# Performance work log

Measured on AMD Instinct MI355X. Metric: run time of the kernel, lower is better.

The kernel has to match this reference:

```python
import jax, jax.numpy as jnp
import numpy as np


def _quat_to_rotT(q):
    # q: [..., 4] in (w, x, y, z) order, exactly mirroring the torch entry order,
    # including the final transpose(3, 2). Returns [..., 3, 3].
    w, x, y, z = q[..., 0], q[..., 1], q[..., 2], q[..., 3]
    R = jnp.stack([
        1.0 - 2.0 * (y ** 2 + z ** 2), 2.0 * x * y - 2.0 * w * z, 2.0 * w * y + 2.0 * x * z,
        2.0 * x * y + 2.0 * z * w, 1.0 - 2.0 * (x ** 2 + z ** 2), -2.0 * w * x + 2.0 * y * z,
        -2.0 * w * y + 2.0 * x * z, 2.0 * w * x + 2.0 * y * z, 1.0 - 2.0 * (x ** 2 + y ** 2),
    ], axis=-1).reshape(q.shape[:-1] + (3, 3))
    return jnp.swapaxes(R, -1, -2)


def _forward(pred_t, pred_r, pred_c, target_r, target_t, model_points, choose, symmetric, diameters, rot_anchors):
    bs, num_rot, _ = pred_r.shape
    # --- anchor regularization: cos_dist = bmm(pred_r, rot_anchors^T) ---
    cos_dist = jnp.einsum('brq,aq->bra', pred_r, rot_anchors)  # [bs, R, R]
    diag = jnp.diagonal(cos_dist, axis1=1, axis2=2)             # [bs, R]
    reg = jnp.max(cos_dist, axis=2) - diag
    loss_reg = jnp.mean(jnp.where(reg > 0.001, reg, 0.0))       # F.threshold(x, 0.001, 0)

    # --- rotate model points by every anchor-refined rotation ---
    rotT = _quat_to_rotT(pred_r)                                 # [bs, R, 3, 3]
    mp = model_points[:, 0]                                      # [bs, N, 3]
    pred_pts = jnp.einsum('bnk,brkj->brnj', mp, rotT)            # [bs, R, N, 3]
    tgt = target_r[:, 0]                                         # [bs, M, 3]

    # symmetric branch: pairwise distances via the |a|^2+|b|^2-2ab expansion
    # (avoids materializing the [bs,R,N,M,3] difference tensor; dist tensor only)
    a2 = jnp.sum(pred_pts ** 2, axis=-1)                         # [bs, R, N]
    b2 = jnp.sum(tgt ** 2, axis=-1)                              # [bs, M]
    ab = jnp.einsum('brnk,bmk->brnm', pred_pts, tgt)             # [bs, R, N, M]
    d2 = a2[:, :, :, None] + b2[:, None, None, :] - 2.0 * ab
    dist_pair = jnp.sqrt(jnp.maximum(d2, 1e-12))
    sym_d = jnp.mean(jnp.min(dist_pair, axis=3), axis=2)         # [bs, R]

    # non-symmetric branch: pointwise distance (M == N)
    nonsym_d = jnp.mean(
        jnp.linalg.norm(pred_pts - tgt[:, None, :, :], axis=-1), axis=2)  # [bs, R]

    d = jnp.where(symmetric[:, None], sym_d, nonsym_d)           # [bs, R]
    per_anchor = d / (diameters[:, None] * pred_c) + jnp.log(pred_c)
    loss_r = jnp.sum(jnp.mean(per_anchor, axis=1))               # summed over batch (torch +=)

    # --- translation smooth-L1 against sampled dense field ---
    tflat = jnp.transpose(target_t, (0, 2, 3, 1)).reshape(bs, -1, 3)      # [bs, H*W, 3]
    tsamp = jnp.take_along_axis(tflat, choose[:, :, None], axis=1)        # [bs, n_sel, 3]
    diff_t = pred_t - tsamp
    ad = jnp.abs(diff_t)
    loss_t = jnp.mean(jnp.where(ad < 1.0, 0.5 * diff_t ** 2, ad - 0.5))

    total = loss_r + 2.0 * loss_reg + 5.0 * loss_t
    return total, loss_r, loss_reg, loss_t


def setup_inputs() -> dict:
    key = jax.random.key(0)
    ks = jax.random.split(key, 8)
    bs, num_rot, N, H, W = 8, 60, 500, 80, 80
    pred_t = jax.random.normal(ks[0], (bs, N, 3), jnp.float32)
    pred_r = jax.random.normal(ks[1], (bs, num_rot, 4), jnp.float32)
    pred_c = jax.random.uniform(ks[2], (bs, num_rot), jnp.float32, 0.05, 1.0)
    target_r = jax.random.normal(ks[3], (bs, 1, N, 3), jnp.float32)
    target_t = jax.random.normal(ks[4], (bs, 3, H, W), jnp.float32)
    model_points = jax.random.normal(ks[5], (bs, 1, N, 3), jnp.float32)
    choose = jax.random.randint(ks[6], (bs, N), 0, H * W)
    symmetric = jnp.ones((bs,), dtype=bool)
    diameters = jnp.ones((bs,), jnp.float32)
    rot_anchors = jax.random.normal(ks[7], (num_rot, 4), jnp.float32)
    return {
        'pred_t': pred_t, 'pred_r': pred_r, 'pred_c': pred_c,
        'target_r': target_r, 'target_t': target_t, 'model_points': model_points,
        'choose': choose, 'symmetric': symmetric, 'diameters': diameters,
        'rot_anchors': rot_anchors,
    }


def reference(pred_t, pred_r, pred_c, target_r, target_t, model_points, choose, symmetric, diameters, rot_anchors):
    return _forward(pred_t, pred_r, pred_c, target_r, target_t, model_points,
                    choose, symmetric, diameters, rot_anchors)
```

## Files before the change

kernel.cpp:

```cpp
#include <hip/hip_runtime.h>
#include <math.h>

#define BS 8
#define NR 60
#define NP 500
#define NHW 6400
#define NBLK (BS*NR)
#define NT_ELEMS (BS*NP*3)
#define LT_PER_BLK 25

__global__ __launch_bounds__(256) void main_kernel(
    const float* __restrict__ pred_t,
    const float* __restrict__ pred_r,
    const float* __restrict__ target_r,
    const float* __restrict__ target_t,
    const float* __restrict__ model_points,
    const int*   __restrict__ choose,
    const float* __restrict__ rot_anchors,
    float* __restrict__ out_sym,
    float* __restrict__ out_non,
    float* __restrict__ out_reg,
    float* __restrict__ out_lt)
{
    const int bid = blockIdx.x;
    const int b = bid / NR;
    const int r = bid % NR;
    const int tid = threadIdx.x;

    __shared__ float4 t4s[NP];
    __shared__ float red[8];

    for (int i = tid; i < NP; i += 256) {
        const float* p = target_r + (b * NP + i) * 3;
        float x = p[0], y = p[1], z = p[2];
        t4s[i] = make_float4(x, y, z, x * x + y * y + z * z);
    }

    const float* q = pred_r + bid * 4;
    const float w = q[0], x = q[1], y = q[2], z = q[3];
    const float r00 = 1.f - 2.f * (y * y + z * z);
    const float r01 = 2.f * x * y - 2.f * w * z;
    const float r02 = 2.f * w * y + 2.f * x * z;
    const float r10 = 2.f * x * y + 2.f * z * w;
    const float r11 = 1.f - 2.f * (x * x + z * z);
    const float r12 = -2.f * w * x + 2.f * y * z;
    const float r20 = -2.f * w * y + 2.f * x * z;
    const float r21 = 2.f * w * x + 2.f * y * z;
    const float r22 = 1.f - 2.f * (x * x + y * y);

    float lt = 0.f;
    if (tid < LT_PER_BLK) {
        int e = bid * LT_PER_BLK + tid;
        int bb = e / 1500;
        int rem = e - bb * 1500;
        int n = rem / 3;
        int k = rem - n * 3;
        int pos = choose[bb * NP + n];
        float ts = target_t[(bb * 3 + k) * NHW + pos];
        float diff = pred_t[e] - ts;
        float ad = fabsf(diff);
        lt = (ad < 1.f) ? 0.5f * diff * diff : ad - 0.5f;
    }

    if (tid < 64) {
        float dot = -3.4e38f;
        if (tid < NR) {
            const float* an = rot_anchors + tid * 4;
            dot = w * an[0] + x * an[1] + y * an[2] + z * an[3];
        }
        float diag = __shfl(dot, r, 64);
        float mx = dot;
        for (int o = 32; o > 0; o >>= 1) mx = fmaxf(mx, __shfl_down(mx, o, 64));
        for (int o = 32; o > 0; o >>= 1) lt += __shfl_down(lt, o, 64);
        if (tid == 0) {
            float rg = mx - diag;
            out_reg[bid] = (rg > 0.001f) ? rg : 0.f;
            out_lt[bid] = lt;
        }
    }

    const int n0 = tid;
    const int n1 = tid + 256;
    const bool has1 = (n1 < NP);

    const float* mpb = model_points + b * NP * 3;
    float m0x = mpb[n0 * 3 + 0], m0y = mpb[n0 * 3 + 1], m0z = mpb[n0 * 3 + 2];
    float m1x = 0.f, m1y = 0.f, m1z = 0.f;
    if (has1) { m1x = mpb[n1 * 3 + 0]; m1y = mpb[n1 * 3 + 1]; m1z = mpb[n1 * 3 + 2]; }

    const float p0x = r00 * m0x + r01 * m0y + r02 * m0z;
    const float p0y = r10 * m0x + r11 * m0y + r12 * m0z;
    const float p0z = r20 * m0x + r21 * m0y + r22 * m0z;
    const float p1x = r00 * m1x + r01 * m1y + r02 * m1z;
    const float p1y = r10 * m1x + r11 * m1y + r12 * m1z;
    const float p1z = r20 * m1x + r21 * m1y + r22 * m1z;
    const float a20 = p0x * p0x + p0y * p0y + p0z * p0z;
    const float a21 = p1x * p1x + p1y * p1y + p1z * p1z;

    __syncthreads();

    float mn0A = 3.4e38f, mn0B = 3.4e38f, mn0C = 3.4e38f, mn0D = 3.4e38f;
    float mn1A = 3.4e38f, mn1B = 3.4e38f, mn1C = 3.4e38f, mn1D = 3.4e38f;
    for (int m = 0; m < NP; m += 4) {
        float4 tA = t4s[m + 0];
        float4 tB = t4s[m + 1];
        float4 tC = t4s[m + 2];
        float4 tD = t4s[m + 3];
        float d0A = fmaf(p0x, tA.x, fmaf(p0y, tA.y, p0z * tA.z));
        float d0B = fmaf(p0x, tB.x, fmaf(p0y, tB.y, p0z * tB.z));
        float d0C = fmaf(p0x, tC.x, fmaf(p0y, tC.y, p0z * tC.z));
        float d0D = fmaf(p0x, tD.x, fmaf(p0y, tD.y, p0z * tD.z));
        float d1A = fmaf(p1x, tA.x, fmaf(p1y, tA.y, p1z * tA.z));
        float d1B = fmaf(p1x, tB.x, fmaf(p1y, tB.y, p1z * tB.z));
        float d1C = fmaf(p1x, tC.x, fmaf(p1y, tC.y, p1z * tC.z));
        float d1D = fmaf(p1x, tD.x, fmaf(p1y, tD.y, p1z * tD.z));
        mn0A = fminf(mn0A, fmaf(-2.f, d0A, tA.w));
        mn0B = fminf(mn0B, fmaf(-2.f, d0B, tB.w));
        mn0C = fminf(mn0C, fmaf(-2.f, d0C, tC.w));
        mn0D = fminf(mn0D, fmaf(-2.f, d0D, tD.w));
        mn1A = fminf(mn1A, fmaf(-2.f, d1A, tA.w));
        mn1B = fminf(mn1B, fmaf(-2.f, d1B, tB.w));
        mn1C = fminf(mn1C, fmaf(-2.f, d1C, tC.w));
        mn1D = fminf(mn1D, fmaf(-2.f, d1D, tD.w));
    }
    const float mn0 = fminf(fminf(mn0A, mn0B), fminf(mn0C, mn0D));
    const float mn1 = fminf(fminf(mn1A, mn1B), fminf(mn1C, mn1D));

    float ssym = 0.f, snon = 0.f;
    {
        float d2 = fmaxf(a20 + mn0, 1e-12f);
        ssym += sqrtf(d2);
        float4 t = t4s[n0];
        float dx = p0x - t.x, dy = p0y - t.y, dz = p0z - t.z;
        snon += sqrtf(dx * dx + dy * dy + dz * dz);
    }
    if (has1) {
        float d2 = fmaxf(a21 + mn1, 1e-12f);
        ssym += sqrtf(d2);
        float4 t = t4s[n1];
        float dx = p1x - t.x, dy = p1y - t.y, dz = p1z - t.z;
        snon += sqrtf(dx * dx + dy * dy + dz * dz);
    }

    for (int o = 32; o > 0; o >>= 1) {
        ssym += __shfl_down(ssym, o, 64);
        snon += __shfl_down(snon, o, 64);
    }
    const int wv = tid >> 6, ln = tid & 63;
    if (ln == 0) { red[wv] = ssym; red[4 + wv] = snon; }
    __syncthreads();
    if (tid == 0) {
        out_sym[bid] = red[0] + red[1] + red[2] + red[3];
        out_non[bid] = red[4] + red[5] + red[6] + red[7];
    }
}

__global__ __launch_bounds__(256) void finalize_kernel(
    const float* __restrict__ out_sym, const float* __restrict__ out_non,
    const float* __restrict__ out_reg, const float* __restrict__ out_lt,
    const float* __restrict__ pred_c,
    const unsigned char* __restrict__ symU8, const int* __restrict__ symI,
    const float* __restrict__ diam, float* __restrict__ out)
{
    const int tid = threadIdx.x;
    float s_r = 0.f, s_reg = 0.f, s_t = 0.f;
    for (int i = tid; i < NBLK; i += 256) {
        int b = i / NR;
        bool sym = (symU8[b] != 0) || (symI[b] != 0);
        float sum = sym ? out_sym[i] : out_non[i];
        float d = sum * (1.0f / NP);
        float c = pred_c[i];
        s_r += (d / (diam[b] * c) + logf(c)) * (1.0f / NR);
        s_reg += out_reg[i];
        s_t += out_lt[i];
    }
    __shared__ float red[12];
    for (int o = 32; o > 0; o >>= 1) {
        s_r += __shfl_down(s_r, o, 64);
        s_reg += __shfl_down(s_reg, o, 64);
        s_t += __shfl_down(s_t, o, 64);
    }
    const int wv = tid >> 6, ln = tid & 63;
    if (ln == 0) { red[wv] = s_r; red[4 + wv] = s_reg; red[8 + wv] = s_t; }
    __syncthreads();
    if (tid == 0) {
        float lr = red[0] + red[1] + red[2] + red[3];
        float lreg = (red[4] + red[5] + red[6] + red[7]) * (1.0f / NBLK);
        float ltv = (red[8] + red[9] + red[10] + red[11]) * (1.0f / NT_ELEMS);
        out[0] = lr + 2.f * lreg + 5.f * ltv;
        out[1] = lr;
        out[2] = lreg;
        out[3] = ltv;
    }
}

extern "C" void kernel_launch(void* const* d_in, const int* in_sizes, int n_in,
                              void* d_out, int out_size, void* d_ws, size_t ws_size,
                              hipStream_t stream) {
    const float* pred_t       = (const float*)d_in[0];
    const float* pred_r       = (const float*)d_in[1];
    const float* pred_c       = (const float*)d_in[2];
    const float* target_r     = (const float*)d_in[3];
    const float* target_t     = (const float*)d_in[4];
    const float* model_points = (const float*)d_in[5];
    const int*   choose       = (const int*)d_in[6];
    const unsigned char* symU8 = (const unsigned char*)d_in[7];
    const int*   symI         = (const int*)d_in[7];
    const float* diam         = (const float*)d_in[8];
    const float* anchors      = (const float*)d_in[9];
    float* out = (float*)d_out;

    char* ws = (char*)d_ws;
    float* o_sym = (float*)ws;
    float* o_non = o_sym + NBLK;
    float* o_reg = o_non + NBLK;
    float* o_lt  = o_reg + NBLK;

    main_kernel<<<NBLK, 256, 0, stream>>>(pred_t, pred_r, target_r, target_t,
                                          model_points, choose, anchors,
                                          o_sym, o_non, o_reg, o_lt);
    finalize_kernel<<<1, 256, 0, stream>>>(o_sym, o_non, o_reg, o_lt,
                                           pred_c, symU8, symI, diam, out);
}
```

Before: 95.47 us.

## Process two rotations per block to reuse shared target loads

Each block now handles a pair of rotation hypotheses instead of one, so every float4 target point read from shared memory feeds four distance candidates rather than two. The grid shrinks from 480 to 240 blocks, and the reg and translation-loss work is redistributed to match. This cuts LDS traffic and the per-block setup cost per rotation. The price is fewer blocks than the MI355X's compute units and more registers per thread.

```diff
diff --git a/kernel.cpp b/kernel.cpp
--- a/kernel.cpp
+++ b/kernel.cpp
@@ -3,11 +3,15 @@
 
 #define BS 8
 #define NR 60
+#define NRP 30
 #define NP 500
 #define NHW 6400
-#define NBLK (BS*NR)
+#define NPAIR (BS*NR)
+#define NBLK (BS*NRP)
 #define NT_ELEMS (BS*NP*3)
-#define LT_PER_BLK 25
+#define LT_PER_BLK 50
+
+#define BIGF 3.4e38f
 
 __global__ __launch_bounds__(256) void main_kernel(
     const float* __restrict__ pred_t,
@@ -23,12 +27,14 @@
     float* __restrict__ out_lt)
 {
     const int bid = blockIdx.x;
-    const int b = bid / NR;
-    const int r = bid % NR;
+    const int b  = bid / NRP;
+    const int rp = bid % NRP;
+    const int r0 = 2 * rp, r1 = 2 * rp + 1;
+    const int pair0 = b * NR + r0;
     const int tid = threadIdx.x;
 
     __shared__ float4 t4s[NP];
-    __shared__ float red[8];
+    __shared__ float red[16];
 
     for (int i = tid; i < NP; i += 256) {
         const float* p = target_r + (b * NP + i) * 3;
@@ -36,17 +42,29 @@
         t4s[i] = make_float4(x, y, z, x * x + y * y + z * z);
     }
 
-    const float* q = pred_r + bid * 4;
-    const float w = q[0], x = q[1], y = q[2], z = q[3];
-    const float r00 = 1.f - 2.f * (y * y + z * z);
-    const float r01 = 2.f * x * y - 2.f * w * z;
-    const float r02 = 2.f * w * y + 2.f * x * z;
-    const float r10 = 2.f * x * y + 2.f * z * w;
-    const float r11 = 1.f - 2.f * (x * x + z * z);
-    const float r12 = -2.f * w * x + 2.f * y * z;
-    const float r20 = -2.f * w * y + 2.f * x * z;
-    const float r21 = 2.f * w * x + 2.f * y * z;
-    const float r22 = 1.f - 2.f * (x * x + y * y);
+    const float* q0p = pred_r + pair0 * 4;
+    const float w0 = q0p[0], x0 = q0p[1], y0 = q0p[2], z0 = q0p[3];
+    const float w1 = q0p[4], x1 = q0p[5], y1 = q0p[6], z1 = q0p[7];
+
+    const float A00 = 1.f - 2.f * (y0 * y0 + z0 * z0);
+    const float A01 = 2.f * x0 * y0 - 2.f * w0 * z0;
+    const float A02 = 2.f * w0 * y0 + 2.f * x0 * z0;
+    const float A10 = 2.f * x0 * y0 + 2.f * z0 * w0;
+    const float A11 = 1.f - 2.f * (x0 * x0 + z0 * z0);
+    const float A12 = -2.f * w0 * x0 + 2.f * y0 * z0;
+    const float A20 = -2.f * w0 * y0 + 2.f * x0 * z0;
+    const float A21 = 2.f * w0 * x0 + 2.f * y0 * z0;
+    const float A22 = 1.f - 2.f * (x0 * x0 + y0 * y0);
+
+    const float B00 = 1.f - 2.f * (y1 * y1 + z1 * z1);
+    const float B01 = 2.f * x1 * y1 - 2.f * w1 * z1;
+    const float B02 = 2.f * w1 * y1 + 2.f * x1 * z1;
+    const float B10 = 2.f * x1 * y1 + 2.f * z1 * w1;
+    const float B11 = 1.f - 2.f * (x1 * x1 + z1 * z1);
+    const float B12 = -2.f * w1 * x1 + 2.f * y1 * z1;
+    const float B20 = -2.f * w1 * y1 + 2.f * x1 * z1;
+    const float B21 = 2.f * w1 * x1 + 2.f * y1 * z1;
+    const float B22 = 1.f - 2.f * (x1 * x1 + y1 * y1);
 
     float lt = 0.f;
     if (tid < LT_PER_BLK) {
@@ -63,95 +81,115 @@
     }
 
     if (tid < 64) {
-        float dot = -3.4e38f;
+        float dot = -BIGF;
         if (tid < NR) {
             const float* an = rot_anchors + tid * 4;
-            dot = w * an[0] + x * an[1] + y * an[2] + z * an[3];
-        }
-        float diag = __shfl(dot, r, 64);
+            dot = w0 * an[0] + x0 * an[1] + y0 * an[2] + z0 * an[3];
+        }
+        float diag = __shfl(dot, r0, 64);
         float mx = dot;
         for (int o = 32; o > 0; o >>= 1) mx = fmaxf(mx, __shfl_down(mx, o, 64));
         for (int o = 32; o > 0; o >>= 1) lt += __shfl_down(lt, o, 64);
         if (tid == 0) {
             float rg = mx - diag;
-            out_reg[bid] = (rg > 0.001f) ? rg : 0.f;
+            out_reg[pair0] = (rg > 0.001f) ? rg : 0.f;
             out_lt[bid] = lt;
+        }
+    } else if (tid < 128) {
+        int ln = tid - 64;
+        float dot = -BIGF;
+        if (ln < NR) {
+            const float* an = rot_anchors + ln * 4;
+            dot = w1 * an[0] + x1 * an[1] + y1 * an[2] + z1 * an[3];
+        }
+        float diag = __shfl(dot, r1, 64);
+        float mx = dot;
+        for (int o = 32; o > 0; o >>= 1) mx = fmaxf(mx, __shfl_down(mx, o, 64));
+        if (ln == 0) {
+            float rg = mx - diag;
+            out_reg[pair0 + 1] = (rg > 0.001f) ? rg : 0.f;
         }
     }
 
     const int n0 = tid;
     const int n1 = tid + 256;
     const bool has1 = (n1 < NP);
+    const int nc = has1 ? n1 : 0;
 
     const float* mpb = model_points + b * NP * 3;
-    float m0x = mpb[n0 * 3 + 0], m0y = mpb[n0 * 3 + 1], m0z = mpb[n0 * 3 + 2];
-    float m1x = 0.f, m1y = 0.f, m1z = 0.f;
-    if (has1) { m1x = mpb[n1 * 3 + 0]; m1y = mpb[n1 * 3 + 1]; m1z = mpb[n1 * 3 + 2]; }
-
-    const float p0x = r00 * m0x + r01 * m0y + r02 * m0z;
-    const float p0y = r10 * m0x + r11 * m0y + r12 * m0z;
-    const float p0z = r20 * m0x + r21 * m0y + r22 * m0z;
-    const float p1x = r00 * m1x + r01 * m1y + r02 * m1z;
-    const float p1y = r10 * m1x + r11 * m1y + r12 * m1z;
-    const float p1z = r20 * m1x + r21 * m1y + r22 * m1z;
-    const float a20 = p0x * p0x + p0y * p0y + p0z * p0z;
-    const float a21 = p1x * p1x + p1y * p1y + p1z * p1z;
+    const float m0x = mpb[n0 * 3 + 0], m0y = mpb[n0 * 3 + 1], m0z = mpb[n0 * 3 + 2];
+    const float m1x = mpb[nc * 3 + 0], m1y = mpb[nc * 3 + 1], m1z = mpb[nc * 3 + 2];
+
+    const float pA0x = A00 * m0x + A01 * m0y + A02 * m0z;
+    const float pA0y = A10 * m0x + A11 * m0y + A12 * m0z;
+    const float pA0z = A20 * m0x + A21 * m0y + A22 * m0z;
+    const float pA1x = A00 * m1x + A01 * m1y + A02 * m1z;
+    const float pA1y = A10 * m1x + A11 * m1y + A12 * m1z;
+    const float pA1z = A20 * m1x + A21 * m1y + A22 * m1z;
+    const float pB0x = B00 * m0x + B01 * m0y + B02 * m0z;
+    const float pB0y = B10 * m0x + B11 * m0y + B12 * m0z;
+    const float pB0z = B20 * m0x + B21 * m0y + B22 * m0z;
+    const float pB1x = B00 * m1x + B01 * m1y + B02 * m1z;
+    const float pB1y = B10 * m1x + B11 * m1y + B12 * m1z;
+    const float pB1z = B20 * m1x + B21 * m1y + B22 * m1z;
+
+    const float a2A0 = pA0x * pA0x + pA0y * pA0y + pA0z * pA0z;
+    const float a2A1 = pA1x * pA1x + pA1y * pA1y + pA1z * pA1z;
+    const float a2B0 = pB0x * pB0x + pB0y * pB0y + pB0z * pB0z;
+    const float a2B1 = pB1x * pB1x + pB1y * pB1y + pB1z * pB1z;
 
     __syncthreads();
 
-    float mn0A = 3.4e38f, mn0B = 3.4e38f, mn0C = 3.4e38f, mn0D = 3.4e38f;
-    float mn1A = 3.4e38f, mn1B = 3.4e38f, mn1C = 3.4e38f, mn1D = 3.4e38f;
-    for (int m = 0; m < NP; m += 4) {
-        float4 tA = t4s[m + 0];
-        float4 tB = t4s[m + 1];
-        float4 tC = t4s[m + 2];
-        float4 tD = t4s[m + 3];
-        float d0A = fmaf(p0x, tA.x, fmaf(p0y, tA.y, p0z * tA.z));
-        float d0B = fmaf(p0x, tB.x, fmaf(p0y, tB.y, p0z * tB.z));
-        float d0C = fmaf(p0x, tC.x, fmaf(p0y, tC.y, p0z * tC.z));
-        float d0D = fmaf(p0x, tD.x, fmaf(p0y, tD.y, p0z * tD.z));
-        float d1A = fmaf(p1x, tA.x, fmaf(p1y, tA.y, p1z * tA.z));
-        float d1B = fmaf(p1x, tB.x, fmaf(p1y, tB.y, p1z * tB.z));
-        float d1C = fmaf(p1x, tC.x, fmaf(p1y, tC.y, p1z * tC.z));
-        float d1D = fmaf(p1x, tD.x, fmaf(p1y, tD.y, p1z * tD.z));
-        mn0A = fminf(mn0A, fmaf(-2.f, d0A, tA.w));
-        mn0B = fminf(mn0B, fmaf(-2.f, d0B, tB.w));
-        mn0C = fminf(mn0C, fmaf(-2.f, d0C, tC.w));
-        mn0D = fminf(mn0D, fmaf(-2.f, d0D, tD.w));
-        mn1A = fminf(mn1A, fmaf(-2.f, d1A, tA.w));
-        mn1B = fminf(mn1B, fmaf(-2.f, d1B, tB.w));
-        mn1C = fminf(mn1C, fmaf(-2.f, d1C, tC.w));
-        mn1D = fminf(mn1D, fmaf(-2.f, d1D, tD.w));
-    }
-    const float mn0 = fminf(fminf(mn0A, mn0B), fminf(mn0C, mn0D));
-    const float mn1 = fminf(fminf(mn1A, mn1B), fminf(mn1C, mn1D));
-
-    float ssym = 0.f, snon = 0.f;
-    {
-        float d2 = fmaxf(a20 + mn0, 1e-12f);
-        ssym += sqrtf(d2);
-        float4 t = t4s[n0];
-        float dx = p0x - t.x, dy = p0y - t.y, dz = p0z - t.z;
-        snon += sqrtf(dx * dx + dy * dy + dz * dz);
-    }
+    float mnA0 = BIGF, mnA1 = BIGF, mnB0 = BIGF, mnB1 = BIGF;
+#pragma unroll 4
+    for (int m = 0; m < NP; ++m) {
+        float4 t = t4s[m];
+        float dA0 = fmaf(pA0x, t.x, fmaf(pA0y, t.y, pA0z * t.z));
+        float dA1 = fmaf(pA1x, t.x, fmaf(pA1y, t.y, pA1z * t.z));
+        float dB0 = fmaf(pB0x, t.x, fmaf(pB0y, t.y, pB0z * t.z));
+        float dB1 = fmaf(pB1x, t.x, fmaf(pB1y, t.y, pB1z * t.z));
+        mnA0 = fminf(mnA0, fmaf(-2.f, dA0, t.w));
+        mnA1 = fminf(mnA1, fmaf(-2.f, dA1, t.w));
+        mnB0 = fminf(mnB0, fmaf(-2.f, dB0, t.w));
+        mnB1 = fminf(mnB1, fmaf(-2.f, dB1, t.w));
+    }
+
+    float t0x, t0y, t0z, t1x, t1y, t1z;
+    { float4 t = t4s[n0]; t0x = t.x; t0y = t.y; t0z = t.z; }
+    { float4 t = t4s[nc]; t1x = t.x; t1y = t.y; t1z = t.z; }
+
+    float symA = sqrtf(fmaxf(a2A0 + mnA0, 1e-12f));
+    float symB = sqrtf(fmaxf(a2B0 + mnB0, 1e-12f));
+    float dxA = pA0x - t0x, dyA = pA0y - t0y, dzA = pA0z - t0z;
+    float dxB = pB0x - t0x, dyB = pB0y - t0y, dzB = pB0z - t0z;
+    float nonA = sqrtf(dxA * dxA + dyA * dyA + dzA * dzA);
+    float nonB = sqrtf(dxB * dxB + dyB * dyB + dzB * dzB);
     if (has1) {
-        float d2 = fmaxf(a21 + mn1, 1e-12f);
-        ssym += sqrtf(d2);
-        float4 t = t4s[n1];
-        float dx = p1x - t.x, dy = p1y - t.y, dz = p1z - t.z;
-        snon += sqrtf(dx * dx + dy * dy + dz * dz);
+        symA += sqrtf(fmaxf(a2A1 + mnA1, 1e-12f));
+        symB += sqrtf(fmaxf(a2B1 + mnB1, 1e-12f));
+        float ex = pA1x - t1x, ey = pA1y - t1y, ez = pA1z - t1z;
+        nonA += sqrtf(ex * ex + ey * ey + ez * ez);
+        float fx = pB1x - t1x, fy = pB1y - t1y, fz = pB1z - t1z;
+        nonB += sqrtf(fx * fx + fy * fy + fz * fz);
     }
 
     for (int o = 32; o > 0; o >>= 1) {
-        ssym += __shfl_down(ssym, o, 64);
-        snon += __shfl_down(snon, o, 64);
+        symA += __shfl_down(symA, o, 64);
+        symB += __shfl_down(symB, o, 64);
+        nonA += __shfl_down(nonA, o, 64);
+        nonB += __shfl_down(nonB, o, 64);
     }
     const int wv = tid >> 6, ln = tid & 63;
-    if (ln == 0) { red[wv] = ssym; red[4 + wv] = snon; }
+    if (ln == 0) {
+        red[wv] = symA; red[4 + wv] = symB;
+        red[8 + wv] = nonA; red[12 + wv] = nonB;
+    }
     __syncthreads();
     if (tid == 0) {
-        out_sym[bid] = red[0] + red[1] + red[2] + red[3];
-        out_non[bid] = red[4] + red[5] + red[6] + red[7];
+        out_sym[pair0]     = red[0] + red[1] + red[2] + red[3];
+        out_sym[pair0 + 1] = red[4] + red[5] + red[6] + red[7];
+        out_non[pair0]     = red[8] + red[9] + red[10] + red[11];
+        out_non[pair0 + 1] = red[12] + red[13] + red[14] + red[15];
     }
 }
 
@@ -164,7 +202,7 @@
 {
     const int tid = threadIdx.x;
     float s_r = 0.f, s_reg = 0.f, s_t = 0.f;
-    for (int i = tid; i < NBLK; i += 256) {
+    for (int i = tid; i < NPAIR; i += 256) {
         int b = i / NR;
         bool sym = (symU8[b] != 0) || (symI[b] != 0);
         float sum = sym ? out_sym[i] : out_non[i];
@@ -172,7 +210,7 @@
         float c = pred_c[i];
         s_r += (d / (diam[b] * c) + logf(c)) * (1.0f / NR);
         s_reg += out_reg[i];
-        s_t += out_lt[i];
+        if (i < NBLK) s_t += out_lt[i];
     }
     __shared__ float red[12];
     for (int o = 32; o > 0; o >>= 1) {
@@ -185,7 +223,7 @@
     __syncthreads();
     if (tid == 0) {
         float lr = red[0] + red[1] + red[2] + red[3];
-        float lreg = (red[4] + red[5] + red[6] + red[7]) * (1.0f / NBLK);
+        float lreg = (red[4] + red[5] + red[6] + red[7]) * (1.0f / NPAIR);
         float ltv = (red[8] + red[9] + red[10] + red[11]) * (1.0f / NT_ELEMS);
         out[0] = lr + 2.f * lreg + 5.f * ltv;
         out[1] = lr;
@@ -212,9 +250,9 @@
 
     char* ws = (char*)d_ws;
     float* o_sym = (float*)ws;
-    float* o_non = o_sym + NBLK;
-    float* o_reg = o_non + NBLK;
-    float* o_lt  = o_reg + NBLK;
+    float* o_non = o_sym + NPAIR;
+    float* o_reg = o_non + NPAIR;
+    float* o_lt  = o_reg + NPAIR;
 
     main_kernel<<<NBLK, 256, 0, stream>>>(pred_t, pred_r, target_r, target_t,
                                           model_points, choose, anchors,
```

Result: slower. 102.5 us (+7.3%).
